# Kernel tuning notes

Measured on AMD Instinct MI355X. Metric: run time of the kernel, lower is better.

The kernel has to match this reference:

```python
import jax, jax.numpy as jnp
import numpy as np
from jax import lax

EPS = 1e-5  # InstanceNorm2d default eps


def _grid_sample_bilinear(x, grid):
    """F.grid_sample(x, grid, mode='bilinear', padding_mode='zeros', align_corners=True).
    x: [N,C,H,W], grid: [N,H,W,2] with (x,y) in [-1,1]."""
    N, C, H, W = x.shape
    gx = (grid[..., 0] + 1.0) * 0.5 * (W - 1)  # [N,H,W] pixel x
    gy = (grid[..., 1] + 1.0) * 0.5 * (H - 1)  # [N,H,W] pixel y
    x0 = jnp.floor(gx)
    y0 = jnp.floor(gy)
    x1 = x0 + 1.0
    y1 = y0 + 1.0
    wx1 = gx - x0
    wx0 = 1.0 - wx1
    wy1 = gy - y0
    wy0 = 1.0 - wy1
    xf = x.reshape(N, C, H * W)

    def corner(xi, yi, wgt):
        inb = (xi >= 0) & (xi <= W - 1) & (yi >= 0) & (yi <= H - 1)
        xi_c = jnp.clip(xi, 0, W - 1).astype(jnp.int32)
        yi_c = jnp.clip(yi, 0, H - 1).astype(jnp.int32)
        idx = (yi_c * W + xi_c).reshape(N, 1, H * W)
        v = jnp.take_along_axis(xf, idx, axis=2).reshape(N, C, H, W)
        return v * (wgt * inb.astype(x.dtype))[:, None]

    return (corner(x0, y0, wx0 * wy0) + corner(x1, y0, wx1 * wy0)
            + corner(x0, y1, wx0 * wy1) + corner(x1, y1, wx1 * wy1))


def _warp(x, flow):
    N, C, H, W = x.shape
    row = jnp.linspace(-1.0, 1.0, W)  # x coordinates
    col = jnp.linspace(-1.0, 1.0, H)  # y coordinates
    base = jnp.stack(jnp.meshgrid(row, col, indexing='xy'), axis=-1)  # [H,W,2]
    norm = jnp.array([W, H], dtype=x.dtype)  # divide flow-x by W, flow-y by H
    grid = base[None].astype(x.dtype) + jnp.transpose(flow, (0, 2, 3, 1)) / norm
    return _grid_sample_bilinear(x, grid)


def setup_inputs() -> dict:
    key = jax.random.key(0)
    k1, k2, k3, k4 = jax.random.split(key, 4)
    N, C, H, W = 4, 64, 256, 256
    x1 = jax.random.normal(k1, (N, C, H, W), dtype=jnp.float32)
    x2 = jax.random.normal(k2, (N, C, H, W), dtype=jnp.float32)
    dw_w = jax.random.normal(k3, (2 * C, 1, 5, 5), dtype=jnp.float32) * 0.05
    dw_b = jnp.zeros((2 * C,), dtype=jnp.float32)
    pw_w = jax.random.normal(k4, (4, 2 * C, 1, 1), dtype=jnp.float32) * 0.05
    return {"x1": x1, "x2": x2, "dw_w": dw_w, "dw_b": dw_b, "pw_w": pw_w}


def reference(x1, x2, dw_w, dw_b, pw_w):
    y = jnp.concatenate([x1, x2], axis=1)  # [N,2C,H,W]
    C2 = y.shape[1]
    # depthwise 5x5 conv, padding=2
    y = lax.conv_general_dilated(y, dw_w, (1, 1), [(2, 2), (2, 2)],
                                 feature_group_count=C2,
                                 dimension_numbers=('NCHW', 'OIHW', 'NCHW'))
    y = y + dw_b[None, :, None, None]
    # InstanceNorm2d (no affine), biased variance over H,W per sample/channel
    mu = jnp.mean(y, axis=(2, 3), keepdims=True)
    var = jnp.mean(jnp.square(y - mu), axis=(2, 3), keepdims=True)
    y = (y - mu) * lax.rsqrt(var + EPS)
    y = jax.nn.gelu(y, approximate=False)
    # 1x1 conv -> 4 flow channels
    flow = lax.conv_general_dilated(y, pw_w, (1, 1), [(0, 0), (0, 0)],
                                    dimension_numbers=('NCHW', 'OIHW', 'NCHW'))
    f1, f2 = flow[:, :2], flow[:, 2:]
    x1_feat = _warp(x1, f1) - x2
    x2_feat = _warp(x2, f2) - x1
    return (x1_feat, x2_feat)
```

## Files before the change

### kernel.cpp

```cpp
#include <hip/hip_runtime.h>


__device__ __forceinline__ float gelu_exact(float x) {
    return 0.5f * x * (1.0f + erff(x * 0.7071067811865475f));
}

__global__ __launch_bounds__(256) void k_dwconv(
    const float* __restrict__ x1, const float* __restrict__ x2,
    const float* __restrict__ dww, const float* __restrict__ dwb,
    float* __restrict__ y, float* __restrict__ part)
{
    const int bid   = blockIdx.x;
    const int plane = bid >> 4;
    const int tile  = bid & 15;
    const int n     = plane >> 7;
    const int c2    = plane & 127;
    const int t     = threadIdx.x;
    const int R0    = tile << 4;

    const float* src = (c2 < 64)
        ? x1 + ((size_t)(n * 64 + c2) << 16)
        : x2 + ((size_t)(n * 64 + (c2 - 64)) << 16);

    float wv[25];
#pragma unroll
    for (int i = 0; i < 25; ++i) wv[i] = dww[c2 * 25 + i];
    const float bias = dwb[c2];

    __shared__ __align__(16) float rows[20][264];

    if (t < 80) {
        const int r = t >> 2, k = t & 3;
        rows[r][(k < 2) ? k : 256 + k] = 0.0f;
    }
#pragma unroll
    for (int k = 0; k < 5; ++k) {
        const int i  = t + (k << 8);
        const int r  = i >> 6;
        const int g  = i & 63;
        const int gr = R0 - 2 + r;
        float4 v = make_float4(0.f, 0.f, 0.f, 0.f);
        if (gr >= 0 && gr < 256) v = *(const float4*)(src + (gr << 8) + (g << 2));
        float2* dst = (float2*)&rows[r][2 + (g << 2)];
        dst[0] = make_float2(v.x, v.y);
        dst[1] = make_float2(v.z, v.w);
    }
    __syncthreads();

    float* yo = y + ((size_t)plane << 16);
    const int q  = t & 63;
    const int rr = t >> 6;
    float s1 = 0.0f, s2 = 0.0f;

#pragma unroll
    for (int it = 0; it < 4; ++it) {
        const int lr = rr + (it << 2);
        float a0 = bias, a1 = bias, a2 = bias, a3 = bias;
#pragma unroll
        for (int dy = 0; dy < 5; ++dy) {
            const float* R = &rows[lr + dy][q << 2];
            float4 A = *(const float4*)R;
            float4 B = *(const float4*)(R + 4);
            const float w0 = wv[dy*5+0], w1 = wv[dy*5+1], w2 = wv[dy*5+2],
                        w3 = wv[dy*5+3], w4 = wv[dy*5+4];
            a0 = fmaf(w0, A.x, a0); a0 = fmaf(w1, A.y, a0); a0 = fmaf(w2, A.z, a0);
            a0 = fmaf(w3, A.w, a0); a0 = fmaf(w4, B.x, a0);
            a1 = fmaf(w0, A.y, a1); a1 = fmaf(w1, A.z, a1); a1 = fmaf(w2, A.w, a1);
            a1 = fmaf(w3, B.x, a1); a1 = fmaf(w4, B.y, a1);
            a2 = fmaf(w0, A.z, a2); a2 = fmaf(w1, A.w, a2); a2 = fmaf(w2, B.x, a2);
            a2 = fmaf(w3, B.y, a2); a2 = fmaf(w4, B.z, a2);
            a3 = fmaf(w0, A.w, a3); a3 = fmaf(w1, B.x, a3); a3 = fmaf(w2, B.y, a3);
            a3 = fmaf(w3, B.z, a3); a3 = fmaf(w4, B.w, a3);
        }
        *(float4*)(yo + ((R0 + lr) << 8) + (q << 2)) = make_float4(a0, a1, a2, a3);
        s1 += a0 + a1 + a2 + a3;
        s2 = fmaf(a0, a0, s2); s2 = fmaf(a1, a1, s2);
        s2 = fmaf(a2, a2, s2); s2 = fmaf(a3, a3, s2);
    }

#pragma unroll
    for (int off = 32; off > 0; off >>= 1) {
        s1 += __shfl_down(s1, off);
        s2 += __shfl_down(s2, off);
    }
    __shared__ float red[8];
    const int wave = t >> 6;
    if ((t & 63) == 0) { red[wave] = s1; red[4 + wave] = s2; }
    __syncthreads();
    if (t == 0) {
        part[tile * 512 + plane]        = red[0] + red[1] + red[2] + red[3];
        part[8192 + tile * 512 + plane] = red[4] + red[5] + red[6] + red[7];
    }
}

__global__ __launch_bounds__(256) void k_stats(
    const float* __restrict__ part, float* __restrict__ stats)
{
    const int p = blockIdx.x * 256 + threadIdx.x;
    float a = 0.0f, b = 0.0f;
#pragma unroll
    for (int tl = 0; tl < 16; ++tl) {
        a += part[tl * 512 + p];
        b += part[8192 + tl * 512 + p];
    }
    const float mean = a * (1.0f / 65536.0f);
    const float var  = b * (1.0f / 65536.0f) - mean * mean;
    stats[2 * p]     = mean;
    stats[2 * p + 1] = rsqrtf(var + 1e-5f);
}

__global__ __launch_bounds__(256) void k_flow(
    const float* __restrict__ y, const float* __restrict__ stats,
    const float* __restrict__ pww, float* __restrict__ flow)
{
    const int bid = blockIdx.x;
    const int n   = bid >> 6;
    const int t   = threadIdx.x;
    const int p4  = ((bid & 63) << 8) | t;

    __shared__ float sm[128], sr[128], spw[512];
    if (t < 128) {
        sm[t] = stats[(n * 128 + t) * 2];
        sr[t] = stats[(n * 128 + t) * 2 + 1];
    } else {
        const int i = t - 128;
        spw[i]       = pww[i];
        spw[i + 128] = pww[i + 128];
        spw[i + 256] = pww[i + 256];
        spw[i + 384] = pww[i + 384];
    }
    __syncthreads();

    const float4* y4 = (const float4*)y + (((size_t)n * 128) << 14) + p4;
    float4 f0 = make_float4(0,0,0,0), f1 = f0, f2 = f0, f3 = f0;
#pragma unroll 4
    for (int c = 0; c < 128; ++c) {
        float4 v = y4[(size_t)c << 14];
        const float m = sm[c], rs = sr[c];
        const float g0 = gelu_exact((v.x - m) * rs);
        const float g1 = gelu_exact((v.y - m) * rs);
        const float g2 = gelu_exact((v.z - m) * rs);
        const float g3 = gelu_exact((v.w - m) * rs);
        float w;
        w = spw[c];       f0.x = fmaf(w, g0, f0.x); f0.y = fmaf(w, g1, f0.y);
                          f0.z = fmaf(w, g2, f0.z); f0.w = fmaf(w, g3, f0.w);
        w = spw[128 + c]; f1.x = fmaf(w, g0, f1.x); f1.y = fmaf(w, g1, f1.y);
                          f1.z = fmaf(w, g2, f1.z); f1.w = fmaf(w, g3, f1.w);
        w = spw[256 + c]; f2.x = fmaf(w, g0, f2.x); f2.y = fmaf(w, g1, f2.y);
                          f2.z = fmaf(w, g2, f2.z); f2.w = fmaf(w, g3, f2.w);
        w = spw[384 + c]; f3.x = fmaf(w, g0, f3.x); f3.y = fmaf(w, g1, f3.y);
                          f3.z = fmaf(w, g2, f3.z); f3.w = fmaf(w, g3, f3.w);
    }
    float4* F = (float4*)flow;
    const int fi = (n << 14) + p4;
    F[fi]          = f0;
    F[65536 + fi]  = f1;
    F[131072 + fi] = f2;
    F[196608 + fi] = f3;
}

__global__ __launch_bounds__(256) void k_warp(
    const float* __restrict__ x1, const float* __restrict__ x2,
    const float* __restrict__ flow, float* __restrict__ out)
{
    const int bid   = blockIdx.x;
    const int n     = bid >> 10;
    const int chunk = (bid >> 8) & 3;
    const int t     = threadIdx.x;
    const int p     = ((bid & 255) << 8) | t;
    const int h     = p >> 8, w = p & 255;
    const int np    = (n << 16) | p;

    const float fx1 = flow[np];
    const float fy1 = flow[262144 + np];
    const float fx2 = flow[524288 + np];
    const float fy2 = flow[786432 + np];
    const float S = 255.0f / 512.0f;

    float gxa = (float)w + fx1 * S, gya = (float)h + fy1 * S;
    float gxb = (float)w + fx2 * S, gyb = (float)h + fy2 * S;

    int a00, a01, a10, a11, b00, b01, b10, b11;
    float wa00, wa01, wa10, wa11, wb00, wb01, wb10, wb11;
    {
        float x0f = floorf(gxa), y0f = floorf(gya);
        float wx1 = gxa - x0f, wy1 = gya - y0f;
        float wx0 = 1.0f - wx1, wy0 = 1.0f - wy1;
        int ix0 = (int)x0f, iy0 = (int)y0f;
        int ix1 = ix0 + 1,  iy1 = iy0 + 1;
        bool vx0 = (ix0 >= 0) && (ix0 <= 255), vx1 = (ix1 >= 0) && (ix1 <= 255);
        bool vy0 = (iy0 >= 0) && (iy0 <= 255), vy1 = (iy1 >= 0) && (iy1 <= 255);
        int x0c = min(max(ix0, 0), 255), x1c = min(max(ix1, 0), 255);
        int y0c = min(max(iy0, 0), 255), y1c = min(max(iy1, 0), 255);
        a00 = (y0c << 8) | x0c; a01 = (y0c << 8) | x1c;
        a10 = (y1c << 8) | x0c; a11 = (y1c << 8) | x1c;
        wa00 = wx0 * wy0 * ((vx0 && vy0) ? 1.0f : 0.0f);
        wa01 = wx1 * wy0 * ((vx1 && vy0) ? 1.0f : 0.0f);
        wa10 = wx0 * wy1 * ((vx0 && vy1) ? 1.0f : 0.0f);
        wa11 = wx1 * wy1 * ((vx1 && vy1) ? 1.0f : 0.0f);
    }
    {
        float x0f = floorf(gxb), y0f = floorf(gyb);
        float wx1 = gxb - x0f, wy1 = gyb - y0f;
        float wx0 = 1.0f - wx1, wy0 = 1.0f - wy1;
        int ix0 = (int)x0f, iy0 = (int)y0f;
        int ix1 = ix0 + 1,  iy1 = iy0 + 1;
        bool vx0 = (ix0 >= 0) && (ix0 <= 255), vx1 = (ix1 >= 0) && (ix1 <= 255);
        bool vy0 = (iy0 >= 0) && (iy0 <= 255), vy1 = (iy1 >= 0) && (iy1 <= 255);
        int x0c = min(max(ix0, 0), 255), x1c = min(max(ix1, 0), 255);
        int y0c = min(max(iy0, 0), 255), y1c = min(max(iy1, 0), 255);
        b00 = (y0c << 8) | x0c; b01 = (y0c << 8) | x1c;
        b10 = (y1c << 8) | x0c; b11 = (y1c << 8) | x1c;
        wb00 = wx0 * wy0 * ((vx0 && vy0) ? 1.0f : 0.0f);
        wb01 = wx1 * wy0 * ((vx1 && vy0) ? 1.0f : 0.0f);
        wb10 = wx0 * wy1 * ((vx0 && vy1) ? 1.0f : 0.0f);
        wb11 = wx1 * wy1 * ((vx1 && vy1) ? 1.0f : 0.0f);
    }

    const int c0 = chunk << 4;
    const float* P1 = x1 + (((size_t)(n * 64 + c0)) << 16);
    const float* P2 = x2 + (((size_t)(n * 64 + c0)) << 16);
    float* O1 = out + (((size_t)(n * 64 + c0)) << 16) + p;
    float* O2 = out + 16777216 + (((size_t)(n * 64 + c0)) << 16) + p;

#pragma unroll 4
    for (int c = 0; c < 16; ++c) {
        const size_t base = (size_t)c << 16;
        const float* q1 = P1 + base;
        const float* q2 = P2 + base;
        float sA = wa00 * q1[a00] + wa01 * q1[a01] + wa10 * q1[a10] + wa11 * q1[a11];
        float sB = wb00 * q2[b00] + wb01 * q2[b01] + wb10 * q2[b10] + wb11 * q2[b11];
        O1[base] = sA - q2[p];
        O2[base] = sB - q1[p];
    }
}

extern "C" void kernel_launch(void* const* d_in, const int* in_sizes, int n_in,
                              void* d_out, int out_size, void* d_ws, size_t ws_size,
                              hipStream_t stream) {
    const float* x1  = (const float*)d_in[0];
    const float* x2  = (const float*)d_in[1];
    const float* dww = (const float*)d_in[2];
    const float* dwb = (const float*)d_in[3];
    const float* pww = (const float*)d_in[4];
    float* out = (float*)d_out;

    float* wsf   = (float*)d_ws;
    float* stats = wsf;
    float* flow  = wsf + 1024;
    float* part  = wsf + 1024 + 1048576;
    float* y     = out;

    k_dwconv<<<8192, 256, 0, stream>>>(x1, x2, dww, dwb, y, part);
    k_stats<<<2, 256, 0, stream>>>(part, stats);
    k_flow<<<256, 256, 0, stream>>>(y, stats, pww, flow);
    k_warp<<<4096, 256, 0, stream>>>(x1, x2, flow, out);
}
```

Measured before the change: 420.7 us.

## Vectorize warp kernel to four pixels per thread and swizzle block order for XCDs

The warp kernel now has each thread handle four adjacent pixels. Flow, direct-subtract inputs and outputs move as float4, and the grid shrinks to 1024 blocks with launch_bounds occupancy 4. Both the dwconv and warp kernels remap blockIdx so that consecutive work items land on the same XCD (blockIdx & 7), which should improve L2 locality on the multi-die MI355X. The cost is far more registers per thread (32 indices and 32 weights), which risks spills or lower occupancy and fewer waves in flight to hide gather latency.

After: 596.5 us. 41.8% more time.

```diff
diff --git a/kernel.cpp b/kernel.cpp
--- a/kernel.cpp
+++ b/kernel.cpp
@@ -10,9 +10,9 @@
     const float* __restrict__ dww, const float* __restrict__ dwb,
     float* __restrict__ y, float* __restrict__ part)
 {
-    const int bid   = blockIdx.x;
-    const int plane = bid >> 4;
-    const int tile  = bid & 15;
+    const int wid   = ((blockIdx.x & 7) << 10) + (blockIdx.x >> 3);
+    const int plane = wid >> 4;
+    const int tile  = wid & 15;
     const int n     = plane >> 7;
     const int c2    = plane & 127;
     const int t     = threadIdx.x;
@@ -159,32 +159,32 @@
     F[196608 + fi] = f3;
 }
 
-__global__ __launch_bounds__(256) void k_warp(
+__global__ __launch_bounds__(256, 4) void k_warp(
     const float* __restrict__ x1, const float* __restrict__ x2,
     const float* __restrict__ flow, float* __restrict__ out)
 {
-    const int bid   = blockIdx.x;
-    const int n     = bid >> 10;
-    const int chunk = (bid >> 8) & 3;
+    const int wid   = ((blockIdx.x & 7) << 7) + (blockIdx.x >> 3);
+    const int n     = wid >> 8;
+    const int chunk = (wid >> 6) & 3;
+    const int rb    = wid & 63;
     const int t     = threadIdx.x;
-    const int p     = ((bid & 255) << 8) | t;
-    const int h     = p >> 8, w = p & 255;
-    const int np    = (n << 16) | p;
-
-    const float fx1 = flow[np];
-    const float fy1 = flow[262144 + np];
-    const float fx2 = flow[524288 + np];
-    const float fy2 = flow[786432 + np];
-    const float S = 255.0f / 512.0f;
-
-    float gxa = (float)w + fx1 * S, gya = (float)h + fy1 * S;
-    float gxb = (float)w + fx2 * S, gyb = (float)h + fy2 * S;
-
-    int a00, a01, a10, a11, b00, b01, b10, b11;
-    float wa00, wa01, wa10, wa11, wb00, wb01, wb10, wb11;
-    {
-        float x0f = floorf(gxa), y0f = floorf(gya);
-        float wx1 = gxa - x0f, wy1 = gya - y0f;
+    const int p0    = (rb << 10) + (t << 2);
+    const int h     = p0 >> 8;
+    const int w0    = p0 & 255;
+    const int np0   = (n << 16) + p0;
+    const float S   = 255.0f / 512.0f;
+
+    const float4 fxa = *(const float4*)(flow + np0);
+    const float4 fya = *(const float4*)(flow + 262144 + np0);
+    const float4 fxb = *(const float4*)(flow + 524288 + np0);
+    const float4 fyb = *(const float4*)(flow + 786432 + np0);
+
+    int   idxA[4][4], idxB[4][4];
+    float wtA[4][4],  wtB[4][4];
+
+    auto bil = [&](float gx, float gy, int* idx, float* wt) {
+        float x0f = floorf(gx), y0f = floorf(gy);
+        float wx1 = gx - x0f, wy1 = gy - y0f;
         float wx0 = 1.0f - wx1, wy0 = 1.0f - wy1;
         int ix0 = (int)x0f, iy0 = (int)y0f;
         int ix1 = ix0 + 1,  iy1 = iy0 + 1;
@@ -192,46 +192,61 @@
         bool vy0 = (iy0 >= 0) && (iy0 <= 255), vy1 = (iy1 >= 0) && (iy1 <= 255);
         int x0c = min(max(ix0, 0), 255), x1c = min(max(ix1, 0), 255);
         int y0c = min(max(iy0, 0), 255), y1c = min(max(iy1, 0), 255);
-        a00 = (y0c << 8) | x0c; a01 = (y0c << 8) | x1c;
-        a10 = (y1c << 8) | x0c; a11 = (y1c << 8) | x1c;
-        wa00 = wx0 * wy0 * ((vx0 && vy0) ? 1.0f : 0.0f);
-        wa01 = wx1 * wy0 * ((vx1 && vy0) ? 1.0f : 0.0f);
-        wa10 = wx0 * wy1 * ((vx0 && vy1) ? 1.0f : 0.0f);
-        wa11 = wx1 * wy1 * ((vx1 && vy1) ? 1.0f : 0.0f);
-    }
+        idx[0] = (y0c << 8) | x0c; idx[1] = (y0c << 8) | x1c;
+        idx[2] = (y1c << 8) | x0c; idx[3] = (y1c << 8) | x1c;
+        wt[0] = wx0 * wy0 * ((vx0 && vy0) ? 1.0f : 0.0f);
+        wt[1] = wx1 * wy0 * ((vx1 && vy0) ? 1.0f : 0.0f);
+        wt[2] = wx0 * wy1 * ((vx0 && vy1) ? 1.0f : 0.0f);
+        wt[3] = wx1 * wy1 * ((vx1 && vy1) ? 1.0f : 0.0f);
+    };
+
     {
-        float x0f = floorf(gxb), y0f = floorf(gyb);
-        float wx1 = gxb - x0f, wy1 = gyb - y0f;
-        float wx0 = 1.0f - wx1, wy0 = 1.0f - wy1;
-        int ix0 = (int)x0f, iy0 = (int)y0f;
-        int ix1 = ix0 + 1,  iy1 = iy0 + 1;
-        bool vx0 = (ix0 >= 0) && (ix0 <= 255), vx1 = (ix1 >= 0) && (ix1 <= 255);
-        bool vy0 = (iy0 >= 0) && (iy0 <= 255), vy1 = (iy1 >= 0) && (iy1 <= 255);
-        int x0c = min(max(ix0, 0), 255), x1c = min(max(ix1, 0), 255);
-        int y0c = min(max(iy0, 0), 255), y1c = min(max(iy1, 0), 255);
-        b00 = (y0c << 8) | x0c; b01 = (y0c << 8) | x1c;
-        b10 = (y1c << 8) | x0c; b11 = (y1c << 8) | x1c;
-        wb00 = wx0 * wy0 * ((vx0 && vy0) ? 1.0f : 0.0f);
-        wb01 = wx1 * wy0 * ((vx1 && vy0) ? 1.0f : 0.0f);
-        wb10 = wx0 * wy1 * ((vx0 && vy1) ? 1.0f : 0.0f);
-        wb11 = wx1 * wy1 * ((vx1 && vy1) ? 1.0f : 0.0f);
+        const float fx[4] = {fxa.x, fxa.y, fxa.z, fxa.w};
+        const float fy[4] = {fya.x, fya.y, fya.z, fya.w};
+#pragma unroll
+        for (int j = 0; j < 4; ++j)
+            bil((float)(w0 + j) + fx[j] * S, (float)h + fy[j] * S, idxA[j], wtA[j]);
+    }
+    {
+        const float fx[4] = {fxb.x, fxb.y, fxb.z, fxb.w};
+        const float fy[4] = {fyb.x, fyb.y, fyb.z, fyb.w};
+#pragma unroll
+        for (int j = 0; j < 4; ++j)
+            bil((float)(w0 + j) + fx[j] * S, (float)h + fy[j] * S, idxB[j], wtB[j]);
     }
 
     const int c0 = chunk << 4;
-    const float* P1 = x1 + (((size_t)(n * 64 + c0)) << 16);
-    const float* P2 = x2 + (((size_t)(n * 64 + c0)) << 16);
-    float* O1 = out + (((size_t)(n * 64 + c0)) << 16) + p;
-    float* O2 = out + 16777216 + (((size_t)(n * 64 + c0)) << 16) + p;
-
-#pragma unroll 4
+    const float* P1 = x1 + ((size_t)(n * 64 + c0) << 16);
+    const float* P2 = x2 + ((size_t)(n * 64 + c0) << 16);
+    float* O1 = out + ((size_t)(n * 64 + c0) << 16) + p0;
+    float* O2 = out + 16777216 + ((size_t)(n * 64 + c0) << 16) + p0;
+
+#pragma unroll 2
     for (int c = 0; c < 16; ++c) {
         const size_t base = (size_t)c << 16;
         const float* q1 = P1 + base;
         const float* q2 = P2 + base;
-        float sA = wa00 * q1[a00] + wa01 * q1[a01] + wa10 * q1[a10] + wa11 * q1[a11];
-        float sB = wb00 * q2[b00] + wb01 * q2[b01] + wb10 * q2[b10] + wb11 * q2[b11];
-        O1[base] = sA - q2[p];
-        O2[base] = sB - q1[p];
+        float4 d1 = *(const float4*)(q1 + p0);
+        float4 d2 = *(const float4*)(q2 + p0);
+        float4 o1, o2;
+        o1.x = wtA[0][0]*q1[idxA[0][0]] + wtA[0][1]*q1[idxA[0][1]]
+             + wtA[0][2]*q1[idxA[0][2]] + wtA[0][3]*q1[idxA[0][3]] - d2.x;
+        o1.y = wtA[1][0]*q1[idxA[1][0]] + wtA[1][1]*q1[idxA[1][1]]
+             + wtA[1][2]*q1[idxA[1][2]] + wtA[1][3]*q1[idxA[1][3]] - d2.y;
+        o1.z = wtA[2][0]*q1[idxA[2][0]] + wtA[2][1]*q1[idxA[2][1]]
+             + wtA[2][2]*q1[idxA[2][2]] + wtA[2][3]*q1[idxA[2][3]] - d2.z;
+        o1.w = wtA[3][0]*q1[idxA[3][0]] + wtA[3][1]*q1[idxA[3][1]]
+             + wtA[3][2]*q1[idxA[3][2]] + wtA[3][3]*q1[idxA[3][3]] - d2.w;
+        o2.x = wtB[0][0]*q2[idxB[0][0]] + wtB[0][1]*q2[idxB[0][1]]
+             + wtB[0][2]*q2[idxB[0][2]] + wtB[0][3]*q2[idxB[0][3]] - d1.x;
+        o2.y = wtB[1][0]*q2[idxB[1][0]] + wtB[1][1]*q2[idxB[1][1]]
+             + wtB[1][2]*q2[idxB[1][2]] + wtB[1][3]*q2[idxB[1][3]] - d1.y;
+        o2.z = wtB[2][0]*q2[idxB[2][0]] + wtB[2][1]*q2[idxB[2][1]]
+             + wtB[2][2]*q2[idxB[2][2]] + wtB[2][3]*q2[idxB[2][3]] - d1.z;
+        o2.w = wtB[3][0]*q2[idxB[3][0]] + wtB[3][1]*q2[idxB[3][1]]
+             + wtB[3][2]*q2[idxB[3][2]] + wtB[3][3]*q2[idxB[3][3]] - d1.w;
+        *(float4*)(O1 + base) = o1;
+        *(float4*)(O2 + base) = o2;
     }
 }
 
@@ -254,5 +269,5 @@
     k_dwconv<<<8192, 256, 0, stream>>>(x1, x2, dww, dwb, y, part);
     k_stats<<<2, 256, 0, stream>>>(part, stats);
     k_flow<<<256, 256, 0, stream>>>(y, stats, pww, flow);
-    k_warp<<<4096, 256, 0, stream>>>(x1, x2, flow, out);
-}
+    k_warp<<<1024, 256, 0, stream>>>(x1, x2, flow, out);
+}
```

## Split flow channel reduction across thread groups and remap blocks across XCDs

Applied to the files above, without the earlier changes.

k_flow now gives each block 64 pixel-quads and splits the 128-channel reduction over four thread groups that meet through a shared-memory reduction, which grows the grid from 256 to 1024 blocks. The point is to fill the GPU, since the old launch left it badly underoccupied. k_dwconv and k_warp now remap blockIdx so that consecutive logical tiles land on the same XCD under round-robin dispatch, with the aim of better L2 locality for neighbouring tiles. The cost is an extra shared-memory reduction and a barrier in k_flow.

Result: faster. 384.8 us (-8.5%).

```diff
diff --git a/kernel.cpp b/kernel.cpp
--- a/kernel.cpp
+++ b/kernel.cpp
@@ -10,9 +10,9 @@
     const float* __restrict__ dww, const float* __restrict__ dwb,
     float* __restrict__ y, float* __restrict__ part)
 {
-    const int bid   = blockIdx.x;
-    const int plane = bid >> 4;
-    const int tile  = bid & 15;
+    const int wid   = ((blockIdx.x & 7) << 10) + (blockIdx.x >> 3);
+    const int plane = wid >> 4;
+    const int tile  = wid & 15;
     const int n     = plane >> 7;
     const int c2    = plane & 127;
     const int t     = threadIdx.x;
@@ -114,11 +114,15 @@
     const float* __restrict__ pww, float* __restrict__ flow)
 {
     const int bid = blockIdx.x;
-    const int n   = bid >> 6;
+    const int n   = bid >> 8;
     const int t   = threadIdx.x;
-    const int p4  = ((bid & 63) << 8) | t;
+    const int pix = t & 63;
+    const int cg  = t >> 6;
+    const int p4  = ((bid & 255) << 6) | pix;
 
     __shared__ float sm[128], sr[128], spw[512];
+    __shared__ __align__(16) float4 acc[64][17];
+
     if (t < 128) {
         sm[t] = stats[(n * 128 + t) * 2];
         sr[t] = stats[(n * 128 + t) * 2 + 1];
@@ -131,43 +135,61 @@
     }
     __syncthreads();
 
-    const float4* y4 = (const float4*)y + (((size_t)n * 128) << 14) + p4;
+    const int cbase = cg << 5;
+    const float4* y4 = (const float4*)y + (((size_t)(n * 128 + cbase)) << 14) + p4;
     float4 f0 = make_float4(0,0,0,0), f1 = f0, f2 = f0, f3 = f0;
 #pragma unroll 4
-    for (int c = 0; c < 128; ++c) {
+    for (int c = 0; c < 32; ++c) {
         float4 v = y4[(size_t)c << 14];
-        const float m = sm[c], rs = sr[c];
+        const int cc = cbase + c;
+        const float m = sm[cc], rs = sr[cc];
         const float g0 = gelu_exact((v.x - m) * rs);
         const float g1 = gelu_exact((v.y - m) * rs);
         const float g2 = gelu_exact((v.z - m) * rs);
         const float g3 = gelu_exact((v.w - m) * rs);
         float w;
-        w = spw[c];       f0.x = fmaf(w, g0, f0.x); f0.y = fmaf(w, g1, f0.y);
-                          f0.z = fmaf(w, g2, f0.z); f0.w = fmaf(w, g3, f0.w);
-        w = spw[128 + c]; f1.x = fmaf(w, g0, f1.x); f1.y = fmaf(w, g1, f1.y);
-                          f1.z = fmaf(w, g2, f1.z); f1.w = fmaf(w, g3, f1.w);
-        w = spw[256 + c]; f2.x = fmaf(w, g0, f2.x); f2.y = fmaf(w, g1, f2.y);
-                          f2.z = fmaf(w, g2, f2.z); f2.w = fmaf(w, g3, f2.w);
-        w = spw[384 + c]; f3.x = fmaf(w, g0, f3.x); f3.y = fmaf(w, g1, f3.y);
-                          f3.z = fmaf(w, g2, f3.z); f3.w = fmaf(w, g3, f3.w);
-    }
-    float4* F = (float4*)flow;
-    const int fi = (n << 14) + p4;
-    F[fi]          = f0;
-    F[65536 + fi]  = f1;
-    F[131072 + fi] = f2;
-    F[196608 + fi] = f3;
+        w = spw[cc];       f0.x = fmaf(w, g0, f0.x); f0.y = fmaf(w, g1, f0.y);
+                           f0.z = fmaf(w, g2, f0.z); f0.w = fmaf(w, g3, f0.w);
+        w = spw[128 + cc]; f1.x = fmaf(w, g0, f1.x); f1.y = fmaf(w, g1, f1.y);
+                           f1.z = fmaf(w, g2, f1.z); f1.w = fmaf(w, g3, f1.w);
+        w = spw[256 + cc]; f2.x = fmaf(w, g0, f2.x); f2.y = fmaf(w, g1, f2.y);
+                           f2.z = fmaf(w, g2, f2.z); f2.w = fmaf(w, g3, f2.w);
+        w = spw[384 + cc]; f3.x = fmaf(w, g0, f3.x); f3.y = fmaf(w, g1, f3.y);
+                           f3.z = fmaf(w, g2, f3.z); f3.w = fmaf(w, g3, f3.w);
+    }
+    acc[pix][(cg << 2) + 0] = f0;
+    acc[pix][(cg << 2) + 1] = f1;
+    acc[pix][(cg << 2) + 2] = f2;
+    acc[pix][(cg << 2) + 3] = f3;
+    __syncthreads();
+
+    if (t < 64) {
+        const int fi = (n << 14) + ((bid & 255) << 6) + t;
+        float4* F = (float4*)flow;
+#pragma unroll
+        for (int j = 0; j < 4; ++j) {
+            float4 a = acc[t][j];
+            float4 b = acc[t][4 + j];
+            float4 c = acc[t][8 + j];
+            float4 d = acc[t][12 + j];
+            float4 s = make_float4(a.x + b.x + c.x + d.x,
+                                   a.y + b.y + c.y + d.y,
+                                   a.z + b.z + c.z + d.z,
+                                   a.w + b.w + c.w + d.w);
+            F[j * 65536 + fi] = s;
+        }
+    }
 }
 
 __global__ __launch_bounds__(256) void k_warp(
     const float* __restrict__ x1, const float* __restrict__ x2,
     const float* __restrict__ flow, float* __restrict__ out)
 {
-    const int bid   = blockIdx.x;
-    const int n     = bid >> 10;
-    const int chunk = (bid >> 8) & 3;
+    const int wid   = ((blockIdx.x & 7) << 9) + (blockIdx.x >> 3);
+    const int n     = wid >> 10;
+    const int chunk = (wid >> 8) & 3;
     const int t     = threadIdx.x;
-    const int p     = ((bid & 255) << 8) | t;
+    const int p     = ((wid & 255) << 8) | t;
     const int h     = p >> 8, w = p & 255;
     const int np    = (n << 16) | p;
 
@@ -218,10 +240,10 @@
     }
 
     const int c0 = chunk << 4;
-    const float* P1 = x1 + (((size_t)(n * 64 + c0)) << 16);
-    const float* P2 = x2 + (((size_t)(n * 64 + c0)) << 16);
-    float* O1 = out + (((size_t)(n * 64 + c0)) << 16) + p;
-    float* O2 = out + 16777216 + (((size_t)(n * 64 + c0)) << 16) + p;
+    const float* P1 = x1 + ((size_t)(n * 64 + c0) << 16);
+    const float* P2 = x2 + ((size_t)(n * 64 + c0) << 16);
+    float* O1 = out + ((size_t)(n * 64 + c0) << 16) + p;
+    float* O2 = out + 16777216 + ((size_t)(n * 64 + c0) << 16) + p;
 
 #pragma unroll 4
     for (int c = 0; c < 16; ++c) {
@@ -253,6 +275,6 @@
 
     k_dwconv<<<8192, 256, 0, stream>>>(x1, x2, dww, dwb, y, part);
     k_stats<<<2, 256, 0, stream>>>(part, stats);
-    k_flow<<<256, 256, 0, stream>>>(y, stats, pww, flow);
+    k_flow<<<1024, 256, 0, stream>>>(y, stats, pww, flow);
     k_warp<<<4096, 256, 0, stream>>>(x1, x2, flow, out);
 }
```
